# Performance work log

Measured on AMD Instinct MI355X. Metric: run time of the kernel, lower is better.

Reference implementation:

```python
import jax, jax.numpy as jnp
import numpy as np

NEG_SLOPE = 0.1

def _leaky(x):
    return jnp.where(x >= 0, x, NEG_SLOPE * x)

def setup_inputs() -> dict:
    key = jax.random.key(0)
    ks = jax.random.split(key, 16)
    B, N, H, W, C = 4, 128, 32, 32, 64
    inp = {
        "image": jax.random.normal(ks[0], (B, 3, H, W), dtype=jnp.float32),
        "coords": jax.random.uniform(ks[1], (B, N, 2), dtype=jnp.float32),
        "w1": jax.random.normal(ks[2], (C, 7), dtype=jnp.float32) * 0.2,
        "b1": jax.random.normal(ks[3], (C,), dtype=jnp.float32) * 0.05,
        "w2": jax.random.normal(ks[4], (C, C), dtype=jnp.float32) * 0.1,
        "b2": jax.random.normal(ks[5], (C,), dtype=jnp.float32) * 0.05,
        "w3": jax.random.normal(ks[6], (C, C), dtype=jnp.float32) * 0.1,
        "b3": jax.random.normal(ks[7], (C,), dtype=jnp.float32) * 0.05,
        "w4": jax.random.normal(ks[8], (C, C), dtype=jnp.float32) * 0.1,
        "b4": jax.random.normal(ks[9], (C,), dtype=jnp.float32) * 0.05,
        "w5": jax.random.normal(ks[10], (C, C), dtype=jnp.float32) * 0.1,
        "b5": jax.random.normal(ks[11], (C,), dtype=jnp.float32) * 0.05,
        "wl": jax.random.normal(ks[12], (3, C), dtype=jnp.float32) * 0.1,
        "bl": jax.random.normal(ks[13], (3,), dtype=jnp.float32) * 0.05,
    }
    return inp

def reference(image, coords, w1, b1, w2, b2, w3, b3, w4, b4, w5, b5, wl, bl):
    B, C_img, H, W = image.shape
    _, N, D = coords.shape
    # position encoding: channel 0 = row/(H-1), channel 1 = col/(W-1)
    row = (jnp.arange(H, dtype=jnp.float32) / (H - 1))[:, None] * jnp.ones((1, W), jnp.float32)
    col = jnp.ones((H, 1), jnp.float32) * (jnp.arange(W, dtype=jnp.float32) / (W - 1))[None, :]
    pos = jnp.stack([row, col], axis=0)  # [2,H,W]
    # x5: [B,5,H,W] = image ++ pos
    x5 = jnp.concatenate([image, jnp.broadcast_to(pos[None], (B, 2, H, W))], axis=1)
    # First 1x1 conv: split weight into image/pos part (5 ch) and coord part (2 ch);
    # avoids materializing the expanded [B*N,7,H,W] input (same math as conv on concat).
    img_part = jnp.einsum('oc,bchw->bohw', w1[:, :5], x5)          # [B,c,H,W]
    crd_part = jnp.einsum('od,bnd->bno', w1[:, 5:], coords)         # [B,N,c]
    h = _leaky(img_part[:, None] + crd_part[:, :, :, None, None] + b1[None, None, :, None, None])  # [B,N,c,H,W]
    for wi, bi in ((w2, b2), (w3, b3), (w4, b4), (w5, b5)):
        h = _leaky(jnp.einsum('oc,bnchw->bnohw', wi, h) + bi[None, None, :, None, None])
    pooled = jnp.mean(h, axis=(-2, -1))                             # [B,N,c] (AdaptiveAvgPool2d(1,1)+Flatten)
    pred = jax.nn.sigmoid(jnp.einsum('oc,bnc->bno', wl, pooled) + bl)  # [B,N,3]
    return jnp.transpose(pred, (0, 2, 1))                           # [B,3,N]
```

## Files before the change

### kernel.cpp

```cpp
#include <hip/hip_runtime.h>
#include <math.h>


typedef float  f32x4  __attribute__((ext_vector_type(4)));
typedef f32x4  f32x4a __attribute__((may_alias));
typedef __bf16 bf16x4 __attribute__((ext_vector_type(4)));
typedef bf16x4 bf16x4a __attribute__((may_alias));
typedef short  s16x4  __attribute__((ext_vector_type(4)));
typedef float  floata __attribute__((may_alias));

static __device__ __forceinline__ f32x4 MFMA16(bf16x4 a, bf16x4 b, f32x4 c) {
    return __builtin_amdgcn_mfma_f32_16x16x16bf16_1k(
        __builtin_bit_cast(s16x4, a), __builtin_bit_cast(s16x4, b), c, 0, 0, 0);
}

static __device__ __forceinline__ bf16x4 cvt4(f32x4 v) {
    bf16x4 r;
    r[0] = (__bf16)v[0]; r[1] = (__bf16)v[1];
    r[2] = (__bf16)v[2]; r[3] = (__bf16)v[3];
    return r;
}

__global__ __launch_bounds__(256, 2) void mlp_mfma_kernel(
    const float* __restrict__ image,
    const float* __restrict__ coords,
    const float* __restrict__ w1, const float* __restrict__ b1,
    const float* __restrict__ w2, const float* __restrict__ b2,
    const float* __restrict__ w3, const float* __restrict__ b3,
    const float* __restrict__ w4, const float* __restrict__ b4,
    const float* __restrict__ w5, const float* __restrict__ b5,
    const float* __restrict__ wl, const float* __restrict__ bl,
    float* __restrict__ out)
{
    __shared__ __align__(16) __bf16 WF[16384];
    __shared__ __align__(16) float  POOL[4][1024];
    __shared__ float BL[320];

    const int tid  = threadIdx.x;
    const int wave = tid >> 6;
    const int lane = tid & 63;
    const int c15  = lane & 15;
    const int q    = lane >> 4;
    const int bn   = blockIdx.x;
    const int b    = bn >> 7;

    const float* Ws[4] = {w2, w3, w4, w5};

    {
        const float* Wsrc = Ws[wave];
        #pragma unroll
        for (int f = 0; f < 16; ++f) {
            const int mt = f >> 2, ks = f & 3;
            f32x4 v = *(const f32x4a*)(Wsrc + (mt * 16 + c15) * 64 + ks * 16 + 4 * q);
            *(bf16x4a*)&WF[((wave * 16 + f) * 64 + lane) * 4] = cvt4(v);
        }
    }
    if (tid < 64) {
        BL[tid]       = b1[tid];
        BL[64 + tid]  = b2[tid];
        BL[128 + tid] = b3[tid];
        BL[192 + tid] = b4[tid];
        BL[256 + tid] = b5[tid];
    }
    __syncthreads();

    bf16x4 wf[4][4][4];
    #pragma unroll
    for (int l = 0; l < 4; ++l)
        #pragma unroll
        for (int mt = 0; mt < 4; ++mt)
            #pragma unroll
            for (int ks = 0; ks < 4; ++ks)
                wf[l][mt][ks] = *(const bf16x4a*)
                    &WF[((l * 16 + mt * 4 + ks) * 64 + lane) * 4];

    bf16x4 a1[4];
    #pragma unroll
    for (int mt = 0; mt < 4; ++mt)
        #pragma unroll
        for (int j = 0; j < 4; ++j) {
            const int k = 4 * q + j;
            float v = (k < 7) ? w1[(mt * 16 + c15) * 7 + k] : 0.0f;
            a1[mt][j] = (__bf16)v;
        }

    const float cx = coords[2 * bn + 0];
    const float cy = coords[2 * bn + 1];
    const float* img = image + b * 3072;

    const float inv31 = 1.0f / 31.0f;
    const bool  q0  = (q == 0);
    const float g0e = (q == 1) ? (float)c15 * inv31        : 0.0f;
    const float g0o = (q == 1) ? (float)(c15 + 16) * inv31 : 0.0f;
    const float g1  = (q == 1) ? cx : 0.0f;
    const float g2  = (q == 1) ? cy : 0.0f;

    f32x4 pool[4];
    #pragma unroll
    for (int mt = 0; mt < 4; ++mt) pool[mt] = (f32x4){0.f, 0.f, 0.f, 0.f};

    float p0, p1, p2;
    {
        const int hw = wave * 256 + c15;
        p0 = img[hw]; p1 = img[1024 + hw]; p2 = img[2048 + hw];
    }

    #pragma unroll 1
    for (int t = 0; t < 16; ++t) {
        const float rowv = (float)(wave * 8 + (t >> 1)) * inv31;
        const float f0 = q0 ? p0 : ((t & 1) ? g0o : g0e);
        const float f1 = q0 ? p1 : g1;
        const float f2 = q0 ? p2 : g2;
        const float f3 = q0 ? rowv : 0.0f;
        bf16x4 B1;
        B1[0] = (__bf16)f0; B1[1] = (__bf16)f1;
        B1[2] = (__bf16)f2; B1[3] = (__bf16)f3;

        {
            const int tt = (t < 15) ? (t + 1) : 15;
            const int hw = wave * 256 + tt * 16 + c15;
            p0 = img[hw]; p1 = img[1024 + hw]; p2 = img[2048 + hw];
        }

        f32x4 acc[4];
        #pragma unroll
        for (int mt = 0; mt < 4; ++mt)
            acc[mt] = *(const f32x4a*)&BL[mt * 16 + 4 * q];
        #pragma unroll
        for (int mt = 0; mt < 4; ++mt)
            acc[mt] = MFMA16(a1[mt], B1, acc[mt]);

        bf16x4 Bf[4];
        #pragma unroll
        for (int l = 0; l < 4; ++l) {
            #pragma unroll
            for (int mt = 0; mt < 4; ++mt) {
                f32x4 v = acc[mt];
                #pragma unroll
                for (int r = 0; r < 4; ++r) v[r] = fmaxf(v[r], 0.1f * v[r]);
                Bf[mt] = cvt4(v);
            }
            #pragma unroll
            for (int mt = 0; mt < 4; ++mt)
                acc[mt] = *(const f32x4a*)&BL[(l + 1) * 64 + mt * 16 + 4 * q];
            #pragma unroll
            for (int ks = 0; ks < 4; ++ks)
                #pragma unroll
                for (int mt = 0; mt < 4; ++mt)
                    acc[mt] = MFMA16(wf[l][mt][ks], Bf[ks], acc[mt]);
        }

        #pragma unroll
        for (int mt = 0; mt < 4; ++mt)
            #pragma unroll
            for (int r = 0; r < 4; ++r) {
                const float v = acc[mt][r];
                pool[mt][r] += fmaxf(v, 0.1f * v);
            }
    }

    floata* Xf = &POOL[wave][0];
    #pragma unroll
    for (int mt = 0; mt < 4; ++mt)
        #pragma unroll
        for (int r = 0; r < 4; ++r)
            Xf[(mt * 16 + 4 * q + r) * 16 + c15] = pool[mt][r];

    __syncthreads();

    if (tid < 64) {
        const int c = tid;
        float s = 0.0f;
        #pragma unroll
        for (int w = 0; w < 4; ++w) {
            const floata* P = &POOL[w][0];
            #pragma unroll
            for (int c4 = 0; c4 < 4; ++c4) {
                f32x4 v = *(const f32x4a*)&P[c * 16 + c4 * 4];
                s += v[0] + v[1] + v[2] + v[3];
            }
        }
        const float p = s * (1.0f / 1024.0f);
        float s0 = wl[c] * p;
        float s1 = wl[64 + c] * p;
        float s2 = wl[128 + c] * p;
        #pragma unroll
        for (int off = 32; off > 0; off >>= 1) {
            s0 += __shfl_down(s0, off, 64);
            s1 += __shfl_down(s1, off, 64);
            s2 += __shfl_down(s2, off, 64);
        }
        if (c == 0) {
            const int n = bn & 127;
            out[(b * 3 + 0) * 128 + n] = 1.0f / (1.0f + expf(-(bl[0] + s0)));
            out[(b * 3 + 1) * 128 + n] = 1.0f / (1.0f + expf(-(bl[1] + s1)));
            out[(b * 3 + 2) * 128 + n] = 1.0f / (1.0f + expf(-(bl[2] + s2)));
        }
    }
}

extern "C" void kernel_launch(void* const* d_in, const int* in_sizes, int n_in,
                              void* d_out, int out_size, void* d_ws, size_t ws_size,
                              hipStream_t stream) {
    const float* image  = (const float*)d_in[0];
    const float* coords = (const float*)d_in[1];
    const float* w1 = (const float*)d_in[2];
    const float* b1 = (const float*)d_in[3];
    const float* w2 = (const float*)d_in[4];
    const float* b2 = (const float*)d_in[5];
    const float* w3 = (const float*)d_in[6];
    const float* b3 = (const float*)d_in[7];
    const float* w4 = (const float*)d_in[8];
    const float* b4 = (const float*)d_in[9];
    const float* w5 = (const float*)d_in[10];
    const float* b5 = (const float*)d_in[11];
    const float* wl = (const float*)d_in[12];
    const float* bl = (const float*)d_in[13];
    float* out = (float*)d_out;

    mlp_mfma_kernel<<<dim3(512), dim3(256), 0, stream>>>(
        image, coords, w1, b1, w2, b2, w3, b3, w4, b4, w5, b5, wl, bl, out);
}
```

Measured before the change: 132.2 us.

## Double block to 512 threads, stream weights from LDS, pool via shuffles

Each block now runs 8 waves that each cover half as many pixel tiles. Every wave no longer keeps all four 64x64 bf16 weight matrices in registers; it reads the A fragments from LDS inside the MFMA loop. This frees registers so more waves fit per CU (launch bounds 512,4). The per-wave pool reduction moves from a large LDS scatter to xor shuffles and a small LDS buffer. In exchange, every MFMA step now needs LDS reads, which may cost bandwidth and add latency.

Result: slower. 319.8 us (+142.0%).

```diff
diff --git a/kernel.cpp b/kernel.cpp
--- a/kernel.cpp
+++ b/kernel.cpp
@@ -7,7 +7,6 @@
 typedef __bf16 bf16x4 __attribute__((ext_vector_type(4)));
 typedef bf16x4 bf16x4a __attribute__((may_alias));
 typedef short  s16x4  __attribute__((ext_vector_type(4)));
-typedef float  floata __attribute__((may_alias));
 
 static __device__ __forceinline__ f32x4 MFMA16(bf16x4 a, bf16x4 b, f32x4 c) {
     return __builtin_amdgcn_mfma_f32_16x16x16bf16_1k(
@@ -21,7 +20,7 @@
     return r;
 }
 
-__global__ __launch_bounds__(256, 2) void mlp_mfma_kernel(
+__global__ __launch_bounds__(512, 4) void mlp_mfma_kernel(
     const float* __restrict__ image,
     const float* __restrict__ coords,
     const float* __restrict__ w1, const float* __restrict__ b1,
@@ -33,7 +32,7 @@
     float* __restrict__ out)
 {
     __shared__ __align__(16) __bf16 WF[16384];
-    __shared__ __align__(16) float  POOL[4][1024];
+    __shared__ __align__(16) float  POOL[8][64];
     __shared__ float BL[320];
 
     const int tid  = threadIdx.x;
@@ -47,12 +46,15 @@
     const float* Ws[4] = {w2, w3, w4, w5};
 
     {
-        const float* Wsrc = Ws[wave];
-        #pragma unroll
-        for (int f = 0; f < 16; ++f) {
+        const int l  = wave >> 1;
+        const int f0 = (wave & 1) * 8;
+        const float* Wsrc = Ws[l];
+        #pragma unroll
+        for (int i = 0; i < 8; ++i) {
+            const int f  = f0 + i;
             const int mt = f >> 2, ks = f & 3;
             f32x4 v = *(const f32x4a*)(Wsrc + (mt * 16 + c15) * 64 + ks * 16 + 4 * q);
-            *(bf16x4a*)&WF[((wave * 16 + f) * 64 + lane) * 4] = cvt4(v);
+            *(bf16x4a*)&WF[((l * 16 + f) * 64 + lane) * 4] = cvt4(v);
         }
     }
     if (tid < 64) {
@@ -64,16 +66,6 @@
     }
     __syncthreads();
 
-    bf16x4 wf[4][4][4];
-    #pragma unroll
-    for (int l = 0; l < 4; ++l)
-        #pragma unroll
-        for (int mt = 0; mt < 4; ++mt)
-            #pragma unroll
-            for (int ks = 0; ks < 4; ++ks)
-                wf[l][mt][ks] = *(const bf16x4a*)
-                    &WF[((l * 16 + mt * 4 + ks) * 64 + lane) * 4];
-
     bf16x4 a1[4];
     #pragma unroll
     for (int mt = 0; mt < 4; ++mt)
@@ -101,13 +93,13 @@
 
     float p0, p1, p2;
     {
-        const int hw = wave * 256 + c15;
+        const int hw = wave * 128 + c15;
         p0 = img[hw]; p1 = img[1024 + hw]; p2 = img[2048 + hw];
     }
 
     #pragma unroll 1
-    for (int t = 0; t < 16; ++t) {
-        const float rowv = (float)(wave * 8 + (t >> 1)) * inv31;
+    for (int t = 0; t < 8; ++t) {
+        const float rowv = (float)(wave * 4 + (t >> 1)) * inv31;
         const float f0 = q0 ? p0 : ((t & 1) ? g0o : g0e);
         const float f1 = q0 ? p1 : g1;
         const float f2 = q0 ? p2 : g2;
@@ -117,8 +109,8 @@
         B1[2] = (__bf16)f2; B1[3] = (__bf16)f3;
 
         {
-            const int tt = (t < 15) ? (t + 1) : 15;
-            const int hw = wave * 256 + tt * 16 + c15;
+            const int tt = (t < 7) ? (t + 1) : 7;
+            const int hw = wave * 128 + tt * 16 + c15;
             p0 = img[hw]; p1 = img[1024 + hw]; p2 = img[2048 + hw];
         }
 
@@ -130,9 +122,9 @@
         for (int mt = 0; mt < 4; ++mt)
             acc[mt] = MFMA16(a1[mt], B1, acc[mt]);
 
-        bf16x4 Bf[4];
         #pragma unroll
         for (int l = 0; l < 4; ++l) {
+            bf16x4 Bf[4];
             #pragma unroll
             for (int mt = 0; mt < 4; ++mt) {
                 f32x4 v = acc[mt];
@@ -144,10 +136,16 @@
             for (int mt = 0; mt < 4; ++mt)
                 acc[mt] = *(const f32x4a*)&BL[(l + 1) * 64 + mt * 16 + 4 * q];
             #pragma unroll
-            for (int ks = 0; ks < 4; ++ks)
+            for (int ks = 0; ks < 4; ++ks) {
+                bf16x4 af[4];
                 #pragma unroll
                 for (int mt = 0; mt < 4; ++mt)
-                    acc[mt] = MFMA16(wf[l][mt][ks], Bf[ks], acc[mt]);
+                    af[mt] = *(const bf16x4a*)
+                        &WF[((l * 16 + mt * 4 + ks) * 64 + lane) * 4];
+                #pragma unroll
+                for (int mt = 0; mt < 4; ++mt)
+                    acc[mt] = MFMA16(af[mt], Bf[ks], acc[mt]);
+            }
         }
 
         #pragma unroll
@@ -159,12 +157,22 @@
             }
     }
 
-    floata* Xf = &POOL[wave][0];
     #pragma unroll
     for (int mt = 0; mt < 4; ++mt)
         #pragma unroll
-        for (int r = 0; r < 4; ++r)
-            Xf[(mt * 16 + 4 * q + r) * 16 + c15] = pool[mt][r];
+        for (int r = 0; r < 4; ++r) {
+            float v = pool[mt][r];
+            v += __shfl_xor(v, 1, 64);
+            v += __shfl_xor(v, 2, 64);
+            v += __shfl_xor(v, 4, 64);
+            v += __shfl_xor(v, 8, 64);
+            pool[mt][r] = v;
+        }
+    if (c15 == 0) {
+        #pragma unroll
+        for (int mt = 0; mt < 4; ++mt)
+            *(f32x4a*)&POOL[wave][mt * 16 + 4 * q] = pool[mt];
+    }
 
     __syncthreads();
 
@@ -172,14 +180,7 @@
         const int c = tid;
         float s = 0.0f;
         #pragma unroll
-        for (int w = 0; w < 4; ++w) {
-            const floata* P = &POOL[w][0];
-            #pragma unroll
-            for (int c4 = 0; c4 < 4; ++c4) {
-                f32x4 v = *(const f32x4a*)&P[c * 16 + c4 * 4];
-                s += v[0] + v[1] + v[2] + v[3];
-            }
-        }
+        for (int w = 0; w < 8; ++w) s += POOL[w][c];
         const float p = s * (1.0f / 1024.0f);
         float s0 = wl[c] * p;
         float s1 = wl[64 + c] * p;
@@ -218,6 +219,6 @@
     const float* bl = (const float*)d_in[13];
     float* out = (float*)d_out;
 
-    mlp_mfma_kernel<<<dim3(512), dim3(256), 0, stream>>>(
+    mlp_mfma_kernel<<<dim3(512), dim3(512), 0, stream>>>(
         image, coords, w1, b1, w2, b2, w3, b3, w4, b4, w5, b5, wl, bl, out);
 }
```
